# Kernel tuning notes

Hardware: AMD Instinct MI355X
Metric: run time of the kernel (lower is better)

## Reference

```python
import jax, jax.numpy as jnp
import numpy as np

N_USERS = 200000
N_ITEMS = 500000
D = 64
N_LAYERS = 3
E = 2000000


def setup_inputs() -> dict:
    key = jax.random.key(0)
    k1, k2, k3, k4 = jax.random.split(key, 4)
    u = jax.random.randint(k1, (E,), 0, N_USERS)
    i = jax.random.randint(k2, (E,), 0, N_ITEMS)
    ua_edges = jnp.stack([u, i], axis=0)  # [2, E] user -> item
    # xavier_uniform bounds for the embedding tables
    bu = float(np.sqrt(6.0 / (N_USERS + D)))
    bi = float(np.sqrt(6.0 / (N_ITEMS + D)))
    user_w = jax.random.uniform(k3, (N_USERS, D), minval=-bu, maxval=bu, dtype=jnp.float32)
    item_w = jax.random.uniform(k4, (N_ITEMS, D), minval=-bi, maxval=bi, dtype=jnp.float32)
    aspect_weight = jnp.array([0.7, 0.3], dtype=jnp.float32)
    return {"ua_edges": ua_edges, "user_w": user_w, "item_w": item_w,
            "aspect_weight": aspect_weight, "n_users": N_USERS}


def _lightgcn_conv(x, row, col, n):
    # degree over targets (col), including self-loops already in row/col
    deg = jax.ops.segment_sum(jnp.ones_like(col, dtype=x.dtype), col, num_segments=n)
    dinv = jnp.where(deg > 0, deg ** -0.5, jnp.zeros_like(deg))
    norm = dinv[row] * dinv[col]                       # [Etot]
    return jax.ops.segment_sum(norm[:, None] * x[row], col, num_segments=n)


def reference(ua_edges, user_w, item_w, aspect_weight, n_users):
    n = user_w.shape[0] + item_w.shape[0]
    src = ua_edges[0]
    dst = ua_edges[1] + n_users
    loops = jnp.arange(n)
    # symmetric bipartite edges + self loops (add_self_loops is idempotent per layer)
    row = jnp.concatenate([src, dst, loops])
    col = jnp.concatenate([dst, src, loops])
    x = jnp.concatenate([user_w, item_w], axis=0)      # [N, D]
    acc = x
    h = x
    for _ in range(N_LAYERS):
        h = _lightgcn_conv(h, row, col, n)
        acc = acc + h
    interest = acc / jnp.asarray(N_LAYERS + 1, x.dtype)  # mean over layer outputs
    alpha = jax.nn.softmax(aspect_weight)
    # raw-tensor edge input has no social graph -> social_emb = user_w
    user_final = alpha[0] * interest[:n_users] + alpha[1] * user_w
    item_final = interest[n_users:]
    return user_final, item_final
```

## Files before the change

### kernel.cpp

```cpp
#include <hip/hip_runtime.h>

#define DD 64
#define BSHIFT 12
#define BNODES (1 << BSHIFT)
#define NBMAX 256

typedef float f32x4 __attribute__((ext_vector_type(4)));
typedef unsigned int u32x2 __attribute__((ext_vector_type(2)));
typedef unsigned int u32;
typedef unsigned short u16;

static inline int cdiv(long long a, int b) { return (int)((a + b - 1) / b); }

__device__ inline f32x4 bf4_to_f(u32x2 v) {
    f32x4 r;
    r.x = __uint_as_float(v.x << 16);
    r.y = __uint_as_float(v.x & 0xFFFF0000u);
    r.z = __uint_as_float(v.y << 16);
    r.w = __uint_as_float(v.y & 0xFFFF0000u);
    return r;
}
__device__ inline u32 pack_bf2(float a, float b) {
    u32 ua = __float_as_uint(a);
    u32 ub = __float_as_uint(b);
    u32 lo = (ua + 0x7FFFu + ((ua >> 16) & 1u)) >> 16;
    u32 hi = (ub + 0x7FFFu + ((ub >> 16) & 1u)) >> 16;
    return lo | (hi << 16);
}
__device__ inline u32x2 pack_bf4(f32x4 v) {
    u32x2 r;
    r.x = pack_bf2(v.x, v.y);
    r.y = pack_bf2(v.z, v.w);
    return r;
}

__global__ void k_zero(int* __restrict__ p, int n) {
    int i = blockIdx.x * blockDim.x + threadIdx.x;
    if (i < n) p[i] = 0;
}

__global__ void k_bhist(const int* __restrict__ edges, int E, int nu,
                        int* __restrict__ bcnt) {
    __shared__ int h[NBMAX];
    int tid = threadIdx.x;
    h[tid] = 0;
    __syncthreads();
    int stride = gridDim.x * blockDim.x;
    for (int e = blockIdx.x * blockDim.x + tid; e < E; e += stride) {
        atomicAdd(&h[edges[e] >> BSHIFT], 1);
        atomicAdd(&h[(nu + edges[E + e]) >> BSHIFT], 1);
    }
    __syncthreads();
    int c = h[tid];
    if (c) atomicAdd(&bcnt[tid], c);
}

__global__ void k_bscan(const int* __restrict__ bcnt, int* __restrict__ bbase,
                        int* __restrict__ bcur, int NB) {
    if (threadIdx.x == 0) {
        int run = 0;
        for (int i = 0; i < NB; i++) { bbase[i] = run; bcur[i] = run; run += bcnt[i]; }
        bbase[NB] = run;
    }
}

__global__ void k_bscatter(const int* __restrict__ edges, int E, int nu,
                           int* __restrict__ bcur, int2* __restrict__ stg,
                           int NB, int CH) {
    __shared__ int h[NBMAX];
    __shared__ int base[NBMAX];
    int tid = threadIdx.x;
    h[tid] = 0;
    __syncthreads();
    int e0 = blockIdx.x * CH;
    int e1 = min(e0 + CH, E);
    for (int e = e0 + tid; e < e1; e += blockDim.x) {
        atomicAdd(&h[edges[e] >> BSHIFT], 1);
        atomicAdd(&h[(nu + edges[E + e]) >> BSHIFT], 1);
    }
    __syncthreads();
    {
        int c = h[tid];
        base[tid] = c ? atomicAdd(&bcur[tid], c) : 0;
        h[tid] = 0;
    }
    __syncthreads();
    for (int e = e0 + tid; e < e1; e += blockDim.x) {
        int u = edges[e];
        int w = nu + edges[E + e];
        int b1 = u >> BSHIFT;
        int b2 = w >> BSHIFT;
        int i1 = atomicAdd(&h[b1], 1);
        stg[base[b1] + i1] = make_int2(u, w);
        int i2 = atomicAdd(&h[b2], 1);
        stg[base[b2] + i2] = make_int2(w, u);
    }
}

__global__ void k_bsort(const int2* __restrict__ stg, const int* __restrict__ bbase,
                        int* __restrict__ adj, int* __restrict__ ptr,
                        float* __restrict__ dinv, int n) {
    __shared__ int cnt[BNODES];
    __shared__ int tsum[256];
    int b = blockIdx.x;
    int tid = threadIdx.x;
    int node0 = b << BSHIFT;
    int s = bbase[b], e = bbase[b + 1];

    for (int i = tid; i < BNODES; i += 256) cnt[i] = 0;
    __syncthreads();
    for (int i = s + tid; i < e; i += 256) {
        int2 r = stg[i];
        atomicAdd(&cnt[r.x - node0], 1);
    }
    __syncthreads();

    int base16 = tid * 16;
    int loc = 0;
#pragma unroll
    for (int j = 0; j < 16; j++) loc += cnt[base16 + j];
    tsum[tid] = loc;
    __syncthreads();
    for (int off = 1; off < 256; off <<= 1) {
        int t = (tid >= off) ? tsum[tid - off] : 0;
        __syncthreads();
        tsum[tid] += t;
        __syncthreads();
    }
    int run = (tid > 0) ? tsum[tid - 1] : 0;
#pragma unroll
    for (int j = 0; j < 16; j++) {
        int node = node0 + base16 + j;
        int c = cnt[base16 + j];
        cnt[base16 + j] = run;
        if (node < n) {
            ptr[node] = s + run;
            dinv[node] = rsqrtf((float)(c + 1));
        }
        run += c;
    }
    __syncthreads();

    for (int i = s + tid; i < e; i += 256) {
        int2 r = stg[i];
        int pos = atomicAdd(&cnt[r.x - node0], 1);
        adj[s + pos] = r.y;
    }
}

__global__ void k_init(const float* __restrict__ uw, const float* __restrict__ iw,
                       const float* __restrict__ dinv, u16* __restrict__ g,
                       int nQuads, int nuQ) {
    int i = blockIdx.x * blockDim.x + threadIdx.x;
    if (i < nQuads) {
        f32x4 x = (i < nuQ) ? ((const f32x4*)uw)[i] : ((const f32x4*)iw)[i - nuQ];
        float s = dinv[i >> 4];
        __builtin_nontemporal_store(pack_bf4(s * x), (u32x2*)g + i);
    }
}

__global__ void k_gatherb(const int* __restrict__ ptr, const int* __restrict__ adj,
                          const float* __restrict__ dinv, const u16* __restrict__ g,
                          u16* __restrict__ gn, int n, int twoE) {
    int t = blockIdx.x * blockDim.x + threadIdx.x;
    int lane = threadIdx.x & 63;
    int j = lane & 15;
    int c = (t >> 6) * 4 + (lane >> 4);
    bool valid = (c < n);
    int cc = valid ? c : (n - 1);
    float dc = dinv[cc];
    int s = ptr[cc];
    int e = (cc == n - 1) ? twoE : ptr[cc + 1];
    int deg = e - s;

    f32x4 acc = bf4_to_f(((const u32x2*)(g + (size_t)cc * DD))[j]);

    int grpbase = lane & 48;
    for (int base = 0; base < deg; base += 16) {
        int cnt = deg - base; if (cnt > 16) cnt = 16;
        int myr = (j < cnt) ? adj[s + base + j] : 0;
        int k = 0;
        for (; k + 4 <= cnt; k += 4) {
            int r0 = __shfl(myr, grpbase + k, 64);
            int r1 = __shfl(myr, grpbase + k + 1, 64);
            int r2 = __shfl(myr, grpbase + k + 2, 64);
            int r3 = __shfl(myr, grpbase + k + 3, 64);
            u32x2 v0 = ((const u32x2*)(g + (size_t)r0 * DD))[j];
            u32x2 v1 = ((const u32x2*)(g + (size_t)r1 * DD))[j];
            u32x2 v2 = ((const u32x2*)(g + (size_t)r2 * DD))[j];
            u32x2 v3 = ((const u32x2*)(g + (size_t)r3 * DD))[j];
            acc += bf4_to_f(v0); acc += bf4_to_f(v1);
            acc += bf4_to_f(v2); acc += bf4_to_f(v3);
        }
        for (; k < cnt; k++) {
            int r = __shfl(myr, grpbase + k, 64);
            acc += bf4_to_f(((const u32x2*)(g + (size_t)r * DD))[j]);
        }
    }

    if (!valid) return;
    f32x4 gnv = (dc * dc) * acc;
    __builtin_nontemporal_store(pack_bf4(gnv), (u32x2*)(gn + (size_t)cc * DD) + j);
}

__global__ void k_gfinal(const int* __restrict__ ptr, const int* __restrict__ adj,
                         const float* __restrict__ dinv, const u16* __restrict__ g2,
                         const u16* __restrict__ g1,
                         const float* __restrict__ uw, const float* __restrict__ iw,
                         const float* __restrict__ aw, float* __restrict__ out,
                         int n, int twoE, int nu) {
    int t = blockIdx.x * blockDim.x + threadIdx.x;
    int lane = threadIdx.x & 63;
    int j = lane & 15;
    int c = (t >> 6) * 4 + (lane >> 4);
    bool valid = (c < n);
    int cc = valid ? c : (n - 1);
    float dc = dinv[cc];
    int s = ptr[cc];
    int e = (cc == n - 1) ? twoE : ptr[cc + 1];
    int deg = e - s;

    f32x4 g2c = bf4_to_f(((const u32x2*)(g2 + (size_t)cc * DD))[j]);
    f32x4 acc = g2c;

    int grpbase = lane & 48;
    for (int base = 0; base < deg; base += 16) {
        int cnt = deg - base; if (cnt > 16) cnt = 16;
        int myr = (j < cnt) ? adj[s + base + j] : 0;
        int k = 0;
        for (; k + 4 <= cnt; k += 4) {
            int r0 = __shfl(myr, grpbase + k, 64);
            int r1 = __shfl(myr, grpbase + k + 1, 64);
            int r2 = __shfl(myr, grpbase + k + 2, 64);
            int r3 = __shfl(myr, grpbase + k + 3, 64);
            u32x2 v0 = ((const u32x2*)(g2 + (size_t)r0 * DD))[j];
            u32x2 v1 = ((const u32x2*)(g2 + (size_t)r1 * DD))[j];
            u32x2 v2 = ((const u32x2*)(g2 + (size_t)r2 * DD))[j];
            u32x2 v3 = ((const u32x2*)(g2 + (size_t)r3 * DD))[j];
            acc += bf4_to_f(v0); acc += bf4_to_f(v1);
            acc += bf4_to_f(v2); acc += bf4_to_f(v3);
        }
        for (; k < cnt; k++) {
            int r = __shfl(myr, grpbase + k, 64);
            acc += bf4_to_f(((const u32x2*)(g2 + (size_t)r * DD))[j]);
        }
    }

    if (!valid) return;
    f32x4 h3 = dc * acc;
    float sq = sqrtf((float)(deg + 1));
    f32x4 h2 = g2c * sq;
    f32x4 h1 = bf4_to_f(((const u32x2*)(g1 + (size_t)cc * DD))[j]) * sq;
    f32x4 x = (c < nu) ? __builtin_nontemporal_load((const f32x4*)(uw + (size_t)c * DD) + j)
                       : __builtin_nontemporal_load((const f32x4*)(iw + (size_t)(c - nu) * DD) + j);
    f32x4 interest = (x + h1 + h2 + h3) * 0.25f;
    f32x4 o;
    if (c < nu) {
        float a0 = aw[0], a1 = aw[1];
        float m = fmaxf(a0, a1);
        float e0 = expf(a0 - m), e1 = expf(a1 - m);
        float al0 = e0 / (e0 + e1);
        o = al0 * interest + (1.0f - al0) * x;
    } else {
        o = interest;
    }
    __builtin_nontemporal_store(o, (f32x4*)(out + (size_t)cc * DD) + j);
}

extern "C" void kernel_launch(void* const* d_in, const int* in_sizes, int n_in,
                              void* d_out, int out_size, void* d_ws, size_t ws_size,
                              hipStream_t stream) {
    const int* edges = (const int*)d_in[0];
    const float* uw = (const float*)d_in[1];
    const float* iw = (const float*)d_in[2];
    const float* aw = (const float*)d_in[3];
    float* out = (float*)d_out;

    const int E = in_sizes[0] / 2;
    const int nu = in_sizes[1] / DD;
    const int ni = in_sizes[2] / DD;
    const int n = nu + ni;
    const int nElem = n * DD;
    const int twoE = 2 * E;
    const int NB = (n + BNODES - 1) >> BSHIFT;

    char* ws = (char*)d_ws;
    size_t off = 0;
    auto alloc = [&](size_t bytes) { size_t r = off; off = (off + bytes + 255) & ~(size_t)255; return r; };
    int* ptr   = (int*)(ws + alloc((size_t)n * 4));
    float* dinv= (float*)(ws + alloc((size_t)n * 4));
    int* adj   = (int*)(ws + alloc((size_t)twoE * 4));
    int* bcnt  = (int*)(ws + alloc(NBMAX * 4));
    int* bbase = (int*)(ws + alloc((NBMAX + 1) * 4));
    int* bcur  = (int*)(ws + alloc(NBMAX * 4));
    u16* g0    = (u16*)(ws + alloc((size_t)nElem * 2));
    u16* g1    = (u16*)(ws + alloc((size_t)nElem * 2));
    size_t g2bytes = (size_t)nElem * 2;
    size_t stbytes = (size_t)twoE * 8;
    u16* g2    = (u16*)(ws + alloc(g2bytes > stbytes ? g2bytes : stbytes));
    int2* stg  = (int2*)g2;

    const int B = 256;
    const int nQuads = nElem / 4;
    const int nuQ = nu * DD / 4;
    const int gI  = cdiv(nQuads, B);
    const int gW4 = cdiv((long long)cdiv(n, 4) * 64, B);
    const int CH  = 4096;
    const int gSC = cdiv(E, CH);

    k_zero<<<1, NBMAX, 0, stream>>>(bcnt, NBMAX);
    k_bhist<<<512, NBMAX, 0, stream>>>(edges, E, nu, bcnt);
    k_bscan<<<1, 64, 0, stream>>>(bcnt, bbase, bcur, NB);
    k_bscatter<<<gSC, NBMAX, 0, stream>>>(edges, E, nu, bcur, stg, NB, CH);
    k_bsort<<<NB, 256, 0, stream>>>(stg, bbase, adj, ptr, dinv, n);

    k_init<<<gI, B, 0, stream>>>(uw, iw, dinv, g0, nQuads, nuQ);

    k_gatherb<<<gW4, B, 0, stream>>>(ptr, adj, dinv, g0, g1, n, twoE);
    k_gatherb<<<gW4, B, 0, stream>>>(ptr, adj, dinv, g1, g2, n, twoE);
    k_gfinal<<<gW4, B, 0, stream>>>(ptr, adj, dinv, g2, g1, uw, iw, aw, out, n, twoE, nu);
}
```

Measured before the change: 590.7 us.

## Pack staging records to 32 bits and process node runs per gather group

Staging records for the bucket sort are packed into one 32-bit word (local node index plus neighbour id), halving scatter/sort traffic. Gather kernels now have each 16-lane group process a run of 16 consecutive nodes, and intermediate stores use normal instead of nontemporal hints so they can stay in cache for the next layer. The final kernel reconstructs the input embedding from the bf16 pre-scaled g0 buffer instead of reading fp32 tables, reducing bytes read at the cost of bf16 precision on the residual term and reduced grid parallelism.

```diff
diff --git a/kernel.cpp b/kernel.cpp
--- a/kernel.cpp
+++ b/kernel.cpp
@@ -4,6 +4,7 @@
 #define BSHIFT 12
 #define BNODES (1 << BSHIFT)
 #define NBMAX 256
+#define RUN 16
 
 typedef float f32x4 __attribute__((ext_vector_type(4)));
 typedef unsigned int u32x2 __attribute__((ext_vector_type(2)));
@@ -65,7 +66,7 @@
 }
 
 __global__ void k_bscatter(const int* __restrict__ edges, int E, int nu,
-                           int* __restrict__ bcur, int2* __restrict__ stg,
+                           int* __restrict__ bcur, u32* __restrict__ stg,
                            int NB, int CH) {
     __shared__ int h[NBMAX];
     __shared__ int base[NBMAX];
@@ -86,18 +87,18 @@
     }
     __syncthreads();
     for (int e = e0 + tid; e < e1; e += blockDim.x) {
-        int u = edges[e];
-        int w = nu + edges[E + e];
+        u32 u = (u32)edges[e];
+        u32 w = (u32)(nu + edges[E + e]);
         int b1 = u >> BSHIFT;
         int b2 = w >> BSHIFT;
         int i1 = atomicAdd(&h[b1], 1);
-        stg[base[b1] + i1] = make_int2(u, w);
+        stg[base[b1] + i1] = ((u & (BNODES - 1)) << 20) | w;
         int i2 = atomicAdd(&h[b2], 1);
-        stg[base[b2] + i2] = make_int2(w, u);
-    }
-}
-
-__global__ void k_bsort(const int2* __restrict__ stg, const int* __restrict__ bbase,
+        stg[base[b2] + i2] = ((w & (BNODES - 1)) << 20) | u;
+    }
+}
+
+__global__ void k_bsort(const u32* __restrict__ stg, const int* __restrict__ bbase,
                         int* __restrict__ adj, int* __restrict__ ptr,
                         float* __restrict__ dinv, int n) {
     __shared__ int cnt[BNODES];
@@ -110,8 +111,7 @@
     for (int i = tid; i < BNODES; i += 256) cnt[i] = 0;
     __syncthreads();
     for (int i = s + tid; i < e; i += 256) {
-        int2 r = stg[i];
-        atomicAdd(&cnt[r.x - node0], 1);
+        atomicAdd(&cnt[stg[i] >> 20], 1);
     }
     __syncthreads();
 
@@ -142,9 +142,9 @@
     __syncthreads();
 
     for (int i = s + tid; i < e; i += 256) {
-        int2 r = stg[i];
-        int pos = atomicAdd(&cnt[r.x - node0], 1);
-        adj[s + pos] = r.y;
+        u32 rec = stg[i];
+        int pos = atomicAdd(&cnt[rec >> 20], 1);
+        adj[s + pos] = (int)(rec & 0xFFFFFu);
     }
 }
 
@@ -155,116 +155,115 @@
     if (i < nQuads) {
         f32x4 x = (i < nuQ) ? ((const f32x4*)uw)[i] : ((const f32x4*)iw)[i - nuQ];
         float s = dinv[i >> 4];
-        __builtin_nontemporal_store(pack_bf4(s * x), (u32x2*)g + i);
+        ((u32x2*)g)[i] = pack_bf4(s * x);
     }
 }
 
 __global__ void k_gatherb(const int* __restrict__ ptr, const int* __restrict__ adj,
                           const float* __restrict__ dinv, const u16* __restrict__ g,
                           u16* __restrict__ gn, int n, int twoE) {
-    int t = blockIdx.x * blockDim.x + threadIdx.x;
     int lane = threadIdx.x & 63;
     int j = lane & 15;
-    int c = (t >> 6) * 4 + (lane >> 4);
-    bool valid = (c < n);
-    int cc = valid ? c : (n - 1);
-    float dc = dinv[cc];
-    int s = ptr[cc];
-    int e = (cc == n - 1) ? twoE : ptr[cc + 1];
-    int deg = e - s;
-
-    f32x4 acc = bf4_to_f(((const u32x2*)(g + (size_t)cc * DD))[j]);
-
+    int wid = (blockIdx.x * blockDim.x + threadIdx.x) >> 6;
+    int c0 = (wid * 4 + (lane >> 4)) * RUN;
     int grpbase = lane & 48;
-    for (int base = 0; base < deg; base += 16) {
-        int cnt = deg - base; if (cnt > 16) cnt = 16;
-        int myr = (j < cnt) ? adj[s + base + j] : 0;
-        int k = 0;
-        for (; k + 4 <= cnt; k += 4) {
-            int r0 = __shfl(myr, grpbase + k, 64);
-            int r1 = __shfl(myr, grpbase + k + 1, 64);
-            int r2 = __shfl(myr, grpbase + k + 2, 64);
-            int r3 = __shfl(myr, grpbase + k + 3, 64);
-            u32x2 v0 = ((const u32x2*)(g + (size_t)r0 * DD))[j];
-            u32x2 v1 = ((const u32x2*)(g + (size_t)r1 * DD))[j];
-            u32x2 v2 = ((const u32x2*)(g + (size_t)r2 * DD))[j];
-            u32x2 v3 = ((const u32x2*)(g + (size_t)r3 * DD))[j];
-            acc += bf4_to_f(v0); acc += bf4_to_f(v1);
-            acc += bf4_to_f(v2); acc += bf4_to_f(v3);
+
+    for (int i = 0; i < RUN; i++) {
+        int c = c0 + i;
+        if (c >= n) break;
+        float dc = dinv[c];
+        int s = ptr[c];
+        int e = (c == n - 1) ? twoE : ptr[c + 1];
+        int deg = e - s;
+
+        f32x4 acc = bf4_to_f(((const u32x2*)(g + (size_t)c * DD))[j]);
+
+        for (int base = 0; base < deg; base += 16) {
+            int cnt = deg - base; if (cnt > 16) cnt = 16;
+            int myr = (j < cnt) ? adj[s + base + j] : 0;
+            int k = 0;
+            for (; k + 4 <= cnt; k += 4) {
+                int r0 = __shfl(myr, grpbase + k, 64);
+                int r1 = __shfl(myr, grpbase + k + 1, 64);
+                int r2 = __shfl(myr, grpbase + k + 2, 64);
+                int r3 = __shfl(myr, grpbase + k + 3, 64);
+                u32x2 v0 = ((const u32x2*)(g + (size_t)r0 * DD))[j];
+                u32x2 v1 = ((const u32x2*)(g + (size_t)r1 * DD))[j];
+                u32x2 v2 = ((const u32x2*)(g + (size_t)r2 * DD))[j];
+                u32x2 v3 = ((const u32x2*)(g + (size_t)r3 * DD))[j];
+                acc += bf4_to_f(v0); acc += bf4_to_f(v1);
+                acc += bf4_to_f(v2); acc += bf4_to_f(v3);
+            }
+            for (; k < cnt; k++) {
+                int r = __shfl(myr, grpbase + k, 64);
+                acc += bf4_to_f(((const u32x2*)(g + (size_t)r * DD))[j]);
+            }
         }
-        for (; k < cnt; k++) {
-            int r = __shfl(myr, grpbase + k, 64);
-            acc += bf4_to_f(((const u32x2*)(g + (size_t)r * DD))[j]);
-        }
-    }
-
-    if (!valid) return;
-    f32x4 gnv = (dc * dc) * acc;
-    __builtin_nontemporal_store(pack_bf4(gnv), (u32x2*)(gn + (size_t)cc * DD) + j);
+
+        f32x4 gnv = (dc * dc) * acc;
+        ((u32x2*)(gn + (size_t)c * DD))[j] = pack_bf4(gnv);
+    }
 }
 
 __global__ void k_gfinal(const int* __restrict__ ptr, const int* __restrict__ adj,
                          const float* __restrict__ dinv, const u16* __restrict__ g2,
-                         const u16* __restrict__ g1,
-                         const float* __restrict__ uw, const float* __restrict__ iw,
+                         const u16* __restrict__ g1, const u16* __restrict__ g0,
                          const float* __restrict__ aw, float* __restrict__ out,
                          int n, int twoE, int nu) {
-    int t = blockIdx.x * blockDim.x + threadIdx.x;
     int lane = threadIdx.x & 63;
     int j = lane & 15;
-    int c = (t >> 6) * 4 + (lane >> 4);
-    bool valid = (c < n);
-    int cc = valid ? c : (n - 1);
-    float dc = dinv[cc];
-    int s = ptr[cc];
-    int e = (cc == n - 1) ? twoE : ptr[cc + 1];
-    int deg = e - s;
-
-    f32x4 g2c = bf4_to_f(((const u32x2*)(g2 + (size_t)cc * DD))[j]);
-    f32x4 acc = g2c;
-
+    int wid = (blockIdx.x * blockDim.x + threadIdx.x) >> 6;
+    int c0 = (wid * 4 + (lane >> 4)) * RUN;
     int grpbase = lane & 48;
-    for (int base = 0; base < deg; base += 16) {
-        int cnt = deg - base; if (cnt > 16) cnt = 16;
-        int myr = (j < cnt) ? adj[s + base + j] : 0;
-        int k = 0;
-        for (; k + 4 <= cnt; k += 4) {
-            int r0 = __shfl(myr, grpbase + k, 64);
-            int r1 = __shfl(myr, grpbase + k + 1, 64);
-            int r2 = __shfl(myr, grpbase + k + 2, 64);
-            int r3 = __shfl(myr, grpbase + k + 3, 64);
-            u32x2 v0 = ((const u32x2*)(g2 + (size_t)r0 * DD))[j];
-            u32x2 v1 = ((const u32x2*)(g2 + (size_t)r1 * DD))[j];
-            u32x2 v2 = ((const u32x2*)(g2 + (size_t)r2 * DD))[j];
-            u32x2 v3 = ((const u32x2*)(g2 + (size_t)r3 * DD))[j];
-            acc += bf4_to_f(v0); acc += bf4_to_f(v1);
-            acc += bf4_to_f(v2); acc += bf4_to_f(v3);
+
+    float a0 = aw[0], a1 = aw[1];
+    float m = fmaxf(a0, a1);
+    float e0 = expf(a0 - m), e1 = expf(a1 - m);
+    float al0 = e0 / (e0 + e1);
+    float al1 = 1.0f - al0;
+
+    for (int i = 0; i < RUN; i++) {
+        int c = c0 + i;
+        if (c >= n) break;
+        float dc = dinv[c];
+        int s = ptr[c];
+        int e = (c == n - 1) ? twoE : ptr[c + 1];
+        int deg = e - s;
+
+        f32x4 g2c = bf4_to_f(((const u32x2*)(g2 + (size_t)c * DD))[j]);
+        f32x4 acc = g2c;
+
+        for (int base = 0; base < deg; base += 16) {
+            int cnt = deg - base; if (cnt > 16) cnt = 16;
+            int myr = (j < cnt) ? adj[s + base + j] : 0;
+            int k = 0;
+            for (; k + 4 <= cnt; k += 4) {
+                int r0 = __shfl(myr, grpbase + k, 64);
+                int r1 = __shfl(myr, grpbase + k + 1, 64);
+                int r2 = __shfl(myr, grpbase + k + 2, 64);
+                int r3 = __shfl(myr, grpbase + k + 3, 64);
+                u32x2 v0 = ((const u32x2*)(g2 + (size_t)r0 * DD))[j];
+                u32x2 v1 = ((const u32x2*)(g2 + (size_t)r1 * DD))[j];
+                u32x2 v2 = ((const u32x2*)(g2 + (size_t)r2 * DD))[j];
+                u32x2 v3 = ((const u32x2*)(g2 + (size_t)r3 * DD))[j];
+                acc += bf4_to_f(v0); acc += bf4_to_f(v1);
+                acc += bf4_to_f(v2); acc += bf4_to_f(v3);
+            }
+            for (; k < cnt; k++) {
+                int r = __shfl(myr, grpbase + k, 64);
+                acc += bf4_to_f(((const u32x2*)(g2 + (size_t)r * DD))[j]);
+            }
         }
-        for (; k < cnt; k++) {
-            int r = __shfl(myr, grpbase + k, 64);
-            acc += bf4_to_f(((const u32x2*)(g2 + (size_t)r * DD))[j]);
-        }
-    }
-
-    if (!valid) return;
-    f32x4 h3 = dc * acc;
-    float sq = sqrtf((float)(deg + 1));
-    f32x4 h2 = g2c * sq;
-    f32x4 h1 = bf4_to_f(((const u32x2*)(g1 + (size_t)cc * DD))[j]) * sq;
-    f32x4 x = (c < nu) ? __builtin_nontemporal_load((const f32x4*)(uw + (size_t)c * DD) + j)
-                       : __builtin_nontemporal_load((const f32x4*)(iw + (size_t)(c - nu) * DD) + j);
-    f32x4 interest = (x + h1 + h2 + h3) * 0.25f;
-    f32x4 o;
-    if (c < nu) {
-        float a0 = aw[0], a1 = aw[1];
-        float m = fmaxf(a0, a1);
-        float e0 = expf(a0 - m), e1 = expf(a1 - m);
-        float al0 = e0 / (e0 + e1);
-        o = al0 * interest + (1.0f - al0) * x;
-    } else {
-        o = interest;
-    }
-    __builtin_nontemporal_store(o, (f32x4*)(out + (size_t)cc * DD) + j);
+
+        f32x4 h3 = dc * acc;
+        float sq = sqrtf((float)(deg + 1));
+        f32x4 xr = bf4_to_f(((const u32x2*)(g0 + (size_t)c * DD))[j]) * sq;
+        f32x4 h1 = bf4_to_f(((const u32x2*)(g1 + (size_t)c * DD))[j]) * sq;
+        f32x4 h2 = g2c * sq;
+        f32x4 interest = (xr + h1 + h2 + h3) * 0.25f;
+        f32x4 o = (c < nu) ? (al0 * interest + al1 * xr) : interest;
+        __builtin_nontemporal_store(o, (f32x4*)(out + (size_t)c * DD) + j);
+    }
 }
 
 extern "C" void kernel_launch(void* const* d_in, const int* in_sizes, int n_in,
@@ -296,17 +295,18 @@
     u16* g0    = (u16*)(ws + alloc((size_t)nElem * 2));
     u16* g1    = (u16*)(ws + alloc((size_t)nElem * 2));
     size_t g2bytes = (size_t)nElem * 2;
-    size_t stbytes = (size_t)twoE * 8;
+    size_t stbytes = (size_t)twoE * 4;
     u16* g2    = (u16*)(ws + alloc(g2bytes > stbytes ? g2bytes : stbytes));
-    int2* stg  = (int2*)g2;
+    u32* stg   = (u32*)g2;
 
     const int B = 256;
     const int nQuads = nElem / 4;
     const int nuQ = nu * DD / 4;
     const int gI  = cdiv(nQuads, B);
-    const int gW4 = cdiv((long long)cdiv(n, 4) * 64, B);
     const int CH  = 4096;
     const int gSC = cdiv(E, CH);
+    const long long nGroups = cdiv(n, RUN);
+    const int gW = cdiv(cdiv(nGroups, 4) * 64, B);
 
     k_zero<<<1, NBMAX, 0, stream>>>(bcnt, NBMAX);
     k_bhist<<<512, NBMAX, 0, stream>>>(edges, E, nu, bcnt);
@@ -316,7 +316,7 @@
 
     k_init<<<gI, B, 0, stream>>>(uw, iw, dinv, g0, nQuads, nuQ);
 
-    k_gatherb<<<gW4, B, 0, stream>>>(ptr, adj, dinv, g0, g1, n, twoE);
-    k_gatherb<<<gW4, B, 0, stream>>>(ptr, adj, dinv, g1, g2, n, twoE);
-    k_gfinal<<<gW4, B, 0, stream>>>(ptr, adj, dinv, g2, g1, uw, iw, aw, out, n, twoE, nu);
-}
+    k_gatherb<<<gW, B, 0, stream>>>(ptr, adj, dinv, g0, g1, n, twoE);
+    k_gatherb<<<gW, B, 0, stream>>>(ptr, adj, dinv, g1, g2, n, twoE);
+    k_gfinal<<<gW, B, 0, stream>>>(ptr, adj, dinv, g2, g1, g0, aw, out, n, twoE, nu);
+}
```

Result: slower. 667.1 us (+12.9%).
